# Performance work log

Measured on AMD Instinct MI355X. Metric: run time of the kernel, lower is better.

The kernel has to match this reference:

```python
import jax, jax.numpy as jnp
import numpy as np

E = 8      # n_routed_experts (== n_local)
K = 2      # n_activated_experts (top-k)
DIM = 2048
INTER = 1408
N_SHARED = 2
STD = 0.02


def setup_inputs() -> dict:
    key = jax.random.key(0)
    ks = jax.random.split(key, 9)
    B, S = 2, 2048
    return {
        "x": jax.random.normal(ks[0], (B, S, DIM), dtype=jnp.float32),
        "gate_w": jax.random.normal(ks[1], (E, DIM), dtype=jnp.float32) * STD,
        "router_bias": jnp.zeros((E,), dtype=jnp.float32),
        "W1": jax.random.normal(ks[2], (E, DIM, INTER), dtype=jnp.float32) * STD,
        "W3": jax.random.normal(ks[3], (E, DIM, INTER), dtype=jnp.float32) * STD,
        "W2": jax.random.normal(ks[4], (E, INTER, DIM), dtype=jnp.float32) * STD,
        "sw1": jax.random.normal(ks[5], (N_SHARED * INTER, DIM), dtype=jnp.float32) * STD,
        "sw3": jax.random.normal(ks[6], (N_SHARED * INTER, DIM), dtype=jnp.float32) * STD,
        "sw2": jax.random.normal(ks[7], (DIM, N_SHARED * INTER), dtype=jnp.float32) * STD,
    }


def reference(x, gate_w, router_bias, W1, W3, W2, sw1, sw3, sw2):
    B, S, D = x.shape
    X = x.reshape(-1, D)                       # [T, D]
    T = X.shape[0]

    # ---- Router: sigmoid scores, biased top-k selection, normalized weights
    logits = jnp.einsum('td,ed->te', X, gate_w)          # [T, E] (route_scale == 1.0)
    scores = jax.nn.sigmoid(logits)
    sel = scores + router_bias[None, :]
    _, idx = jax.lax.top_k(sel, K)                       # [T, K] int indices
    w = jnp.take_along_axis(scores, idx, axis=1)         # gather true scores
    w = w / jnp.clip(jnp.sum(w, axis=-1, keepdims=True), 1e-12)

    # Dense combine matrix [T, E]: gate weight where expert selected else 0
    gate_full = jnp.zeros((T, E), dtype=w.dtype).at[jnp.arange(T)[:, None], idx].set(w)

    # ---- Expert MLPs (SwiGLU) computed per-expert, combined by routing weight
    h1 = jnp.einsum('td,edh->eth', X, W1)                # [E, T, INTER]
    h3 = jnp.einsum('td,edh->eth', X, W3)
    y = jnp.einsum('eth,ehd->etd', jax.nn.silu(h1) * h3, W2)  # [E, T, D]
    out = jnp.einsum('etd,te->td', y, gate_full)         # weighted combine

    # ---- Shared expert MLP (always on)
    shared = jnp.einsum('th,dh->td',
                        jax.nn.silu(jnp.einsum('td,hd->th', X, sw1))
                        * jnp.einsum('td,hd->th', X, sw3), sw2)
    out = out + shared
    return out.reshape(B, S, D)
```

## Files before the change

### kernel.cpp

```cpp
#include <hip/hip_runtime.h>

#define DEV __device__ __forceinline__

typedef __attribute__((ext_vector_type(8))) short short8;
typedef __attribute__((ext_vector_type(4))) float floatx4;

constexpr int Tn  = 4096;
constexpr int Dm  = 2048;
constexpr int In  = 1408;
constexpr int En  = 8;
constexpr int SIn = 2816;
constexpr int CAP = 10240;

constexpr int SH_H = (Tn / 256) * (SIn / 128);
constexpr int SH_O = (Tn / 256) * (Dm / 256);
constexpr int NBLK = 256;

DEV unsigned short f2bf(float f) {
  unsigned int u = __float_as_uint(f);
  u += 0x7FFF + ((u >> 16) & 1);
  return (unsigned short)(u >> 16);
}

DEV float bf2f(unsigned short u) {
  return __uint_as_float(((unsigned int)u) << 16);
}

DEV void stg(const char* g, char* l) {
  __builtin_amdgcn_global_load_lds(
      (const __attribute__((address_space(1))) unsigned int*)g,
      (__attribute__((address_space(3))) unsigned int*)l, 16, 0, 0);
}

DEV unsigned ldsoff(const void* p) {
  return (unsigned)(unsigned long long)(__attribute__((address_space(3))) const char*)p;
}

#define BARR()  __builtin_amdgcn_s_barrier()
#define LGKM0() do { asm volatile("s_waitcnt lgkmcnt(0)" ::: "memory"); \
                     __builtin_amdgcn_sched_barrier(0); } while (0)
#define LGKM8() asm volatile("s_waitcnt lgkmcnt(8)" ::: "memory")
#define VMC(n)  asm volatile("s_waitcnt vmcnt(" #n ")" ::: "memory")
#define PRIO(x) __builtin_amdgcn_s_setprio(x)

#define DSR(dst, addr, OFFSTR) \
  asm volatile("ds_read_b128 %0, %1 offset:" OFFSTR : "=v"(dst) : "v"(addr))

#define RDA_LO(af, a) do { \
  DSR(af[0][0], a, "0");     DSR(af[0][1], a, "1024"); \
  DSR(af[1][0], a, "2048");  DSR(af[1][1], a, "3072"); \
  DSR(af[2][0], a, "4096");  DSR(af[2][1], a, "5120"); \
  DSR(af[3][0], a, "6144");  DSR(af[3][1], a, "7168"); } while (0)
#define RDA_HI(af, a) do { \
  DSR(af[0][0], a, "8192");  DSR(af[0][1], a, "9216"); \
  DSR(af[1][0], a, "10240"); DSR(af[1][1], a, "11264"); \
  DSR(af[2][0], a, "12288"); DSR(af[2][1], a, "13312"); \
  DSR(af[3][0], a, "14336"); DSR(af[3][1], a, "15360"); } while (0)
#define RDB_LO(bf, a) do { \
  DSR(bf[0][0], a, "0");    DSR(bf[0][1], a, "1024"); \
  DSR(bf[1][0], a, "2048"); DSR(bf[1][1], a, "3072"); } while (0)
#define RDB_HI(bf, a) do { \
  DSR(bf[2][0], a, "4096"); DSR(bf[2][1], a, "5120"); \
  DSR(bf[3][0], a, "6144"); DSR(bf[3][1], a, "7168"); } while (0)


__global__ void convert_all_kernel(const float* __restrict__ x,
                                   const float* __restrict__ sw1,
                                   const float* __restrict__ sw3,
                                   const float* __restrict__ sw2,
                                   unsigned short* __restrict__ Xb,
                                   unsigned short* __restrict__ sw1b,
                                   unsigned short* __restrict__ sw3b,
                                   unsigned short* __restrict__ sw2b) {
  int y = blockIdx.y;
  const float* src; unsigned short* dst; int n4;
  if (y == 0)      { src = x;   dst = Xb;   n4 = Tn * Dm / 4; }
  else if (y == 1) { src = sw1; dst = sw1b; n4 = SIn * Dm / 4; }
  else if (y == 2) { src = sw3; dst = sw3b; n4 = SIn * Dm / 4; }
  else             { src = sw2; dst = sw2b; n4 = Dm * SIn / 4; }
  int i = blockIdx.x * 256 + threadIdx.x;
  if (i >= n4) return;
  float4 v = ((const float4*)src)[i];
  union { unsigned short u[4]; unsigned long long ll; } p;
  p.u[0] = f2bf(v.x); p.u[1] = f2bf(v.y); p.u[2] = f2bf(v.z); p.u[3] = f2bf(v.w);
  *(unsigned long long*)(dst + (long)i * 4) = p.ll;
}

__global__ void transpose_all_kernel(const float* __restrict__ W1,
                                     const float* __restrict__ W3,
                                     const float* __restrict__ W2,
                                     unsigned short* __restrict__ W1t,
                                     unsigned short* __restrict__ W3t,
                                     unsigned short* __restrict__ W2t) {
  __shared__ float tile[64][65];
  int z = blockIdx.z;
  const float* s0; unsigned short* d0; int R, C;
  if (z == 0)      { s0 = W1; d0 = W1t; R = Dm; C = In; }
  else if (z == 1) { s0 = W3; d0 = W3t; R = Dm; C = In; }
  else             { s0 = W2; d0 = W2t; R = In; C = Dm; }
  int tilesC = C >> 6;
  int tr = (blockIdx.x / tilesC) << 6;
  int tc = (blockIdx.x % tilesC) << 6;
  const float* s = s0 + (long)blockIdx.y * R * C;
  unsigned short* d = d0 + (long)blockIdx.y * R * C;
  int rr = threadIdx.x >> 4, c4 = (threadIdx.x & 15) << 2;
#pragma unroll
  for (int p = 0; p < 4; p++) {
    float4 v = *(const float4*)&s[(long)(tr + rr + 16 * p) * C + tc + c4];
    tile[rr + 16 * p][c4]     = v.x;
    tile[rr + 16 * p][c4 + 1] = v.y;
    tile[rr + 16 * p][c4 + 2] = v.z;
    tile[rr + 16 * p][c4 + 3] = v.w;
  }
  __syncthreads();
  int oc = threadIdx.x >> 5, i2 = (threadIdx.x & 31) << 1;
#pragma unroll
  for (int p = 0; p < 8; p++) {
    int j = oc + 8 * p;
    union { unsigned short u[2]; unsigned int w; } pk;
    pk.u[0] = f2bf(tile[i2][j]);
    pk.u[1] = f2bf(tile[i2 + 1][j]);
    *(unsigned int*)&d[(long)(tc + j) * R + tr + i2] = pk.w;
  }
}


__global__ void init_kernel(int* counts, int* ptok) {
  int i = blockIdx.x * 256 + threadIdx.x;
  if (i < En) counts[i] = 0;
  if (i < CAP) ptok[i] = 0;
}

__global__ void router_kernel(const float* __restrict__ X, const float* __restrict__ GW,
                              const float* __restrict__ bias,
                              int* __restrict__ route_e, float* __restrict__ route_w,
                              int* __restrict__ counts) {
  int t = blockIdx.x, lane = threadIdx.x;
  const float* xr = X + (long)t * Dm;
  double acc[En];
#pragma unroll
  for (int e = 0; e < En; e++) acc[e] = 0.0;
  for (int d = lane; d < Dm; d += 64) {
    double xv = (double)xr[d];
#pragma unroll
    for (int e = 0; e < En; e++) acc[e] += xv * (double)GW[e * Dm + d];
  }
#pragma unroll
  for (int off = 32; off > 0; off >>= 1) {
#pragma unroll
    for (int e = 0; e < En; e++) acc[e] += __shfl_down(acc[e], off);
  }
  if (lane == 0) {
    double sc[En], sel[En];
#pragma unroll
    for (int e = 0; e < En; e++) {
      sc[e] = 1.0 / (1.0 + exp(-acc[e]));
      sel[e] = sc[e] + (double)bias[e];
    }
    int i0 = 0;
#pragma unroll
    for (int e = 1; e < En; e++) if (sel[e] > sel[i0]) i0 = e;
    int i1 = (i0 == 0) ? 1 : 0;
#pragma unroll
    for (int e = 0; e < En; e++) if (e != i0 && sel[e] > sel[i1]) i1 = e;
    double s = sc[i0] + sc[i1];
    if (s < 1e-12) s = 1e-12;
    route_e[t * 2] = i0;  route_e[t * 2 + 1] = i1;
    route_w[t * 2] = (float)(sc[i0] / s);  route_w[t * 2 + 1] = (float)(sc[i1] / s);
    atomicAdd(&counts[i0], 1);  atomicAdd(&counts[i1], 1);
  }
}

__global__ void offsets_kernel(const int* __restrict__ counts,
                               int* __restrict__ offs, int* __restrict__ fill) {
  if (threadIdx.x == 0) {
    int off = 0;
    for (int e = 0; e < En; e++) {
      offs[e] = off; fill[e] = off;
      off += (counts[e] + 255) & ~255;
    }
    offs[En] = off;
  }
}

__global__ void scatter_kernel(const int* __restrict__ re, int* __restrict__ fill,
                               int* __restrict__ pt, int* __restrict__ pslot) {
  int i = blockIdx.x * 256 + threadIdx.x;
  if (i < Tn * 2) {
    int e = re[i];
    int slot = atomicAdd(&fill[e], 1);
    pt[slot] = i >> 1;
    pslot[i] = slot;
  }
}


DEV void mm16(floatx4 (&acc)[8][4], const short8 (&af)[4][2],
              const short8 (&bf)[4][2], int mq, int nq) {
#pragma unroll
  for (int i = 0; i < 4; i++)
#pragma unroll
    for (int n = 0; n < 2; n++)
#pragma unroll
      for (int kk = 0; kk < 2; kk++)
        acc[4 * mq + i][2 * nq + n] = __builtin_amdgcn_mfma_f32_16x16x32_bf16(
            af[i][kk], bf[2 * nq + n][kk], acc[4 * mq + i][2 * nq + n], 0, 0, 0);
}

DEV void chunk_rc(int c, int& rowh, int& colb) {
  rowh = ((c >> 7) << 4) | ((c >> 2) & 15);
  colb = (((c >> 6) & 1) << 6) | ((((c & 3) << 4)) ^ ((c & 32) ? 32 : 0));
}

DEV void gemm_core(char* LDS, const char* (&gA)[2][2], const char* (&gB)[2][2],
                   floatx4 (&acc)[8][4], int NT, int wm, int wn, int wv, int aswz) {
  const int bsel = (wn >> 1) * 16384 + ((wn & 1) << 13);
  const int wb = wv * 1024;
  unsigned base = ldsoff(LDS);
  unsigned aA0 = base + wm * 16384 + aswz;
  unsigned aB0 = base + 32768 + bsel + aswz;
  unsigned aA1 = aA0 + 65536, aB1 = aB0 + 65536;
  stg(gB[0][0], LDS + 32768 + wb);
  stg(gB[1][0], LDS + 32768 + 16384 + wb);
  stg(gB[0][1], LDS + 32768 + 8192 + wb);
  stg(gB[1][1], LDS + 32768 + 16384 + 8192 + wb);
  stg(gA[0][0], LDS + wb);
  stg(gA[1][0], LDS + 16384 + wb);
  stg(gA[0][1], LDS + 8192 + wb);
  stg(gA[1][1], LDS + 16384 + 8192 + wb);
  stg(gA[0][0] + 128, LDS + 65536 + wb);
  stg(gA[1][0] + 128, LDS + 65536 + 16384 + wb);
  stg(gB[0][0] + 128, LDS + 65536 + 32768 + wb);
  stg(gB[1][0] + 128, LDS + 65536 + 32768 + 16384 + wb);
  VMC(4);
  BARR();
  short8 af[4][2], bf[4][2];

  auto tile = [&](int t, int b, unsigned aA, unsigned aB) {
    char* An = LDS + ((b ^ 1) << 16);
    char* Bn = An + 32768;
    char* Ac = LDS + (b << 16);
    char* Bc = Ac + 32768;
    const int kn = (t + 1) << 7, ka = (t + 2) << 7;
    const bool s1 = (t + 1 < NT), s2 = (t + 2 < NT);
    RDA_LO(af, aA); RDB_LO(bf, aB);
    if (s1) { stg(gB[0][1] + kn, Bn + 8192 + wb);
              stg(gB[1][1] + kn, Bn + 16384 + 8192 + wb); }
    LGKM8(); BARR(); LGKM0(); PRIO(1); mm16(acc, af, bf, 0, 0); PRIO(0); BARR();
    RDB_HI(bf, aB);
    if (s1) { stg(gA[0][1] + kn, An + 8192 + wb);
              stg(gA[1][1] + kn, An + 16384 + 8192 + wb); }
    BARR(); LGKM0(); PRIO(1); mm16(acc, af, bf, 0, 1); PRIO(0); BARR();
    RDA_HI(af, aA);
    if (s2) { stg(gA[0][0] + ka, Ac + wb);
              stg(gA[1][0] + ka, Ac + 16384 + wb); }
    BARR(); LGKM0(); PRIO(1); mm16(acc, af, bf, 1, 0); PRIO(0); BARR();
    if (s2) { stg(gB[0][0] + ka, Bc + wb);
              stg(gB[1][0] + ka, Bc + 16384 + wb); }
    BARR(); LGKM0(); PRIO(1); mm16(acc, af, bf, 1, 1); PRIO(0);
    if (s2)      { VMC(4); }
    else if (s1) { VMC(0); }
    BARR();
  };
#pragma unroll 1
  for (int t2 = 0; t2 < NT; t2 += 2) {
    tile(t2, 0, aA0, aB0);
    tile(t2 + 1, 1, aA1, aB1);
  }
}


DEV void h_body(const unsigned short* Xb, const unsigned short* B1p,
                const unsigned short* B3p, unsigned short* ap, int Nact,
                int m0, int n0, const int* ptok, bool routed, char* LDS) {
  int tid = threadIdx.x, wv = tid >> 6, lane = tid & 63;
  int wm = wv >> 2, wn = wv & 3;
  int fr = lane & 15, fq = lane >> 4;
  int aswz = fr * 64 + ((fq * 16) ^ ((fr & 8) << 2));

  const char* gA[2][2]; const char* gB[2][2];
#pragma unroll
  for (int j = 0; j < 2; j++) {
    int rowh, colb;
    chunk_rc(j * 512 + tid, rowh, colb);
#pragma unroll
    for (int h = 0; h < 2; h++) {
      int grA = m0 + h * 128 + rowh;
      long ra = routed ? (long)ptok[grA] : (long)grA;
      gA[h][j] = (const char*)Xb + ra * (long)(Dm * 2) + colb;
      int rt = h * 128 + rowh;
      const unsigned short* src = ((rt >> 5) & 1) ? B3p : B1p;
      long rb = (long)n0 + ((rt >> 6) << 5) + (rt & 31);
      gB[h][j] = (const char*)src + rb * (long)(Dm * 2) + colb;
    }
  }
  floatx4 acc[8][4];
#pragma unroll
  for (int i = 0; i < 8; i++)
#pragma unroll
    for (int n = 0; n < 4; n++) acc[i][n] = (floatx4)0.0f;

  gemm_core(LDS, gA, gB, acc, Dm / 64, wm, wn, wv, aswz);

#pragma unroll
  for (int mi = 0; mi < 8; mi++)
#pragma unroll
    for (int n = 0; n < 2; n++)
#pragma unroll
      for (int r = 0; r < 4; r++) {
        int row = m0 + wm * 128 + mi * 16 + fq * 4 + r;
        int col = n0 + wn * 32 + n * 16 + fr;
        float h1 = acc[mi][n][r], h3 = acc[mi][n + 2][r];
        float v = h1 / (1.0f + __expf(-h1)) * h3;
        ap[(long)row * Nact + col] = f2bf(v);
      }
}

__global__ __launch_bounds__(512, 1)
void h_all(const unsigned short* __restrict__ Xb,
           const unsigned short* __restrict__ W1t,
           const unsigned short* __restrict__ W3t,
           const unsigned short* __restrict__ sw1b,
           const unsigned short* __restrict__ sw3b,
           unsigned short* __restrict__ act,
           unsigned short* __restrict__ actS,
           const int* __restrict__ ptok,
           const int* __restrict__ offs) {
  extern __shared__ char LDS[];
  const int Mr = offs[En] >> 8;
  const int RT = Mr * (In / 128);
  const int TT = RT + SH_H;
#pragma unroll 1
  for (int t = blockIdx.x; t < TT; t += NBLK) {
    if (t < RT) {
      int m0 = (t % Mr) * 256, n0 = (t / Mr) * 128;
      int e = 0;
      while (!(m0 >= offs[e] && m0 < offs[e + 1])) e++;
      h_body(Xb, W1t + (long)e * In * Dm, W3t + (long)e * In * Dm,
             act, In, m0, n0, ptok, true, LDS);
    } else {
      int u = t - RT;
      int m0 = (u & 15) * 256, n0 = (u >> 4) * 128;
      h_body(Xb, sw1b, sw3b, actS, SIn, m0, n0, nullptr, false, LDS);
    }
  }
}


DEV void o_core(const unsigned short* Apt, const unsigned short* Bpt,
                int lda, int ldb, int NT, int m0, int n0,
                floatx4 (&acc)[8][4], char* LDS) {
  int tid = threadIdx.x, wv = tid >> 6, lane = tid & 63;
  int wm = wv >> 2, wn = wv & 3;
  int fr = lane & 15, fq = lane >> 4;
  int aswz = fr * 64 + ((fq * 16) ^ ((fr & 8) << 2));

  const char* gA[2][2]; const char* gB[2][2];
#pragma unroll
  for (int j = 0; j < 2; j++) {
    int rowh, colb;
    chunk_rc(j * 512 + tid, rowh, colb);
#pragma unroll
    for (int h = 0; h < 2; h++) {
      gA[h][j] = (const char*)Apt + (long)(m0 + h * 128 + rowh) * (lda * 2) + colb;
      gB[h][j] = (const char*)Bpt + (long)(n0 + h * 128 + rowh) * (ldb * 2) + colb;
    }
  }
#pragma unroll
  for (int i = 0; i < 8; i++)
#pragma unroll
    for (int n = 0; n < 4; n++) acc[i][n] = (floatx4)0.0f;

  gemm_core(LDS, gA, gB, acc, NT, wm, wn, wv, aswz);
}

__global__ __launch_bounds__(512, 1)
void o_all(const unsigned short* __restrict__ act,
           const unsigned short* __restrict__ actS,
           const unsigned short* __restrict__ W2t,
           const unsigned short* __restrict__ sw2b,
           unsigned short* __restrict__ yR,
           float* __restrict__ out,
           const int* __restrict__ offs) {
  extern __shared__ char LDS[];
  const int Mr = offs[En] >> 8;
  const int RT = Mr * (Dm / 256);
  const int TT = RT + SH_O;
  int lane = threadIdx.x & 63, wv = threadIdx.x >> 6;
  int wm = wv >> 2, wn = wv & 3;
  int fr = lane & 15, fq = lane >> 4;
#pragma unroll 1
  for (int t = blockIdx.x; t < TT; t += NBLK) {
    floatx4 acc[8][4];
    if (t < RT) {
      int m0 = (t % Mr) * 256, n0 = (t / Mr) * 256;
      int e = 0;
      while (!(m0 >= offs[e] && m0 < offs[e + 1])) e++;
      o_core(act, W2t + (long)e * Dm * In, In, In, In / 64, m0, n0, acc, LDS);
#pragma unroll
      for (int mi = 0; mi < 8; mi++)
#pragma unroll
        for (int r = 0; r < 4; r++) {
          int row = m0 + wm * 128 + mi * 16 + fq * 4 + r;
#pragma unroll
          for (int ni = 0; ni < 4; ni++) {
            int col = n0 + wn * 64 + ni * 16 + fr;
            yR[(long)row * Dm + col] = f2bf(acc[mi][ni][r]);
          }
        }
    } else {
      int u = t - RT;
      int m0 = (u & 15) * 256, n0 = (u >> 4) * 256;
      o_core(actS, sw2b, SIn, SIn, SIn / 64, m0, n0, acc, LDS);
#pragma unroll
      for (int mi = 0; mi < 8; mi++)
#pragma unroll
        for (int r = 0; r < 4; r++) {
          int row = m0 + wm * 128 + mi * 16 + fq * 4 + r;
#pragma unroll
          for (int ni = 0; ni < 4; ni++) {
            int col = n0 + wn * 64 + ni * 16 + fr;
            out[(long)row * Dm + col] = acc[mi][ni][r];
          }
        }
    }
  }
}


__global__ void combine_kernel(const unsigned short* __restrict__ yR,
                               const int* __restrict__ pslot,
                               const float* __restrict__ rw,
                               float* __restrict__ out) {
  int idx = blockIdx.x * 256 + threadIdx.x;
  int t = idx >> 9, c4 = idx & 511;
  int s0 = pslot[t * 2], s1 = pslot[t * 2 + 1];
  float w0 = rw[t * 2], w1 = rw[t * 2 + 1];
  ushort4 a = ((const ushort4*)(yR + (long)s0 * Dm))[c4];
  ushort4 b = ((const ushort4*)(yR + (long)s1 * Dm))[c4];
  float4* op = (float4*)(out + (long)t * Dm) + c4;
  float4 o = *op;
  o.x += w0 * bf2f(a.x) + w1 * bf2f(b.x);
  o.y += w0 * bf2f(a.y) + w1 * bf2f(b.y);
  o.z += w0 * bf2f(a.z) + w1 * bf2f(b.z);
  o.w += w0 * bf2f(a.w) + w1 * bf2f(b.w);
  *op = o;
}


extern "C" void kernel_launch(void* const* d_in, const int* in_sizes, int n_in,
                              void* d_out, int out_size, void* d_ws, size_t ws_size,
                              hipStream_t stream) {
  const float* x    = (const float*)d_in[0];
  const float* gw   = (const float*)d_in[1];
  const float* bias = (const float*)d_in[2];
  const float* W1   = (const float*)d_in[3];
  const float* W3   = (const float*)d_in[4];
  const float* W2   = (const float*)d_in[5];
  const float* sw1  = (const float*)d_in[6];
  const float* sw3  = (const float*)d_in[7];
  const float* sw2  = (const float*)d_in[8];
  float* out = (float*)d_out;

  static bool attr_done = false;
  if (!attr_done) {
    hipFuncSetAttribute(reinterpret_cast<const void*>(h_all),
                        hipFuncAttributeMaxDynamicSharedMemorySize, 131072);
    hipFuncSetAttribute(reinterpret_cast<const void*>(o_all),
                        hipFuncAttributeMaxDynamicSharedMemorySize, 131072);
    attr_done = true;
  }

  char* p = (char*)d_ws;
  auto alloc = [&](size_t bytes) {
    char* r = p; p += (bytes + 255) & ~(size_t)255; return r;
  };
  unsigned short* Xb   = (unsigned short*)alloc((size_t)Tn * Dm * 2);
  unsigned short* W1t  = (unsigned short*)alloc((size_t)En * In * Dm * 2);
  unsigned short* W3t  = (unsigned short*)alloc((size_t)En * In * Dm * 2);
  unsigned short* W2t  = (unsigned short*)alloc((size_t)En * Dm * In * 2);
  unsigned short* sw1b = (unsigned short*)alloc((size_t)SIn * Dm * 2);
  unsigned short* sw3b = (unsigned short*)alloc((size_t)SIn * Dm * 2);
  unsigned short* sw2b = (unsigned short*)alloc((size_t)Dm * SIn * 2);
  unsigned short* act  = (unsigned short*)alloc((size_t)CAP * In * 2);
  unsigned short* actS = (unsigned short*)alloc((size_t)Tn * SIn * 2);
  unsigned short* yR   = (unsigned short*)alloc((size_t)CAP * Dm * 2);
  int*   route_e = (int*)alloc(Tn * 2 * 4);
  float* route_w = (float*)alloc(Tn * 2 * 4);
  int*   counts  = (int*)alloc(256);
  int*   offs    = (int*)alloc(256);
  int*   fill    = (int*)alloc(256);
  int*   ptok    = (int*)alloc(CAP * 4);
  int*   pslot   = (int*)alloc(Tn * 2 * 4);

  convert_all_kernel<<<dim3(Tn * Dm / 4 / 256, 4), 256, 0, stream>>>(
      x, sw1, sw3, sw2, Xb, sw1b, sw3b, sw2b);
  transpose_all_kernel<<<dim3((Dm / 64) * (In / 64), En, 3), 256, 0, stream>>>(
      W1, W3, W2, W1t, W3t, W2t);

  init_kernel<<<(CAP + 255) / 256, 256, 0, stream>>>(counts, ptok);
  router_kernel<<<Tn, 64, 0, stream>>>(x, gw, bias, route_e, route_w, counts);
  offsets_kernel<<<1, 1, 0, stream>>>(counts, offs, fill);
  scatter_kernel<<<Tn * 2 / 256, 256, 0, stream>>>(route_e, fill, ptok, pslot);

  h_all<<<NBLK, 512, 131072, stream>>>(Xb, W1t, W3t, sw1b, sw3b, act, actS, ptok, offs);
  o_all<<<NBLK, 512, 131072, stream>>>(act, actS, W2t, sw2b, yR, out, offs);
  combine_kernel<<<Tn * (Dm / 4) / 256, 256, 0, stream>>>(yR, pslot, route_w, out);
}
```

Baseline: 832.5 us.

## Fuse prep kernels, merge offsets/scatter, and remap tile schedule per XCD

Merges the convert, transpose, router and init kernels into one prep kernel with block ranges, and replaces counts/offsets/scatter with a single-block LDS-based offscatter kernel. This cuts kernel launches and the global atomics. The h_all and o_all tile loops now give each XCD a contiguous chunk of tiles to improve L2 locality, and o_all schedules shared-expert tiles first. The single-block scatter serializes work, and the contiguous chunking may unbalance load across XCDs.

```diff
diff --git a/kernel.cpp b/kernel.cpp
--- a/kernel.cpp
+++ b/kernel.cpp
@@ -15,6 +15,19 @@
 constexpr int SH_H = (Tn / 256) * (SIn / 128);
 constexpr int SH_O = (Tn / 256) * (Dm / 256);
 constexpr int NBLK = 256;
+
+constexpr int RB  = Tn / 4;
+constexpr int IB  = CAP / 256;
+constexpr int CXB = Tn * Dm / 4 / 256;
+constexpr int CWB = SIn * Dm / 4 / 256;
+constexpr int TBZ = (Dm / 64) * (In / 64);
+constexpr int O1 = RB;
+constexpr int O2 = O1 + IB;
+constexpr int O3 = O2 + CXB;
+constexpr int O4 = O3 + CWB;
+constexpr int O5 = O4 + CWB;
+constexpr int O6 = O5 + CWB;
+constexpr int PREP_B = O6 + TBZ * En * 3;
 
 DEV unsigned short f2bf(float f) {
   unsigned int u = __float_as_uint(f);
@@ -64,45 +77,96 @@
   DSR(bf[3][0], a, "6144"); DSR(bf[3][1], a, "7168"); } while (0)
 
 
-__global__ void convert_all_kernel(const float* __restrict__ x,
-                                   const float* __restrict__ sw1,
-                                   const float* __restrict__ sw3,
-                                   const float* __restrict__ sw2,
-                                   unsigned short* __restrict__ Xb,
-                                   unsigned short* __restrict__ sw1b,
-                                   unsigned short* __restrict__ sw3b,
-                                   unsigned short* __restrict__ sw2b) {
-  int y = blockIdx.y;
-  const float* src; unsigned short* dst; int n4;
-  if (y == 0)      { src = x;   dst = Xb;   n4 = Tn * Dm / 4; }
-  else if (y == 1) { src = sw1; dst = sw1b; n4 = SIn * Dm / 4; }
-  else if (y == 2) { src = sw3; dst = sw3b; n4 = SIn * Dm / 4; }
-  else             { src = sw2; dst = sw2b; n4 = Dm * SIn / 4; }
-  int i = blockIdx.x * 256 + threadIdx.x;
-  if (i >= n4) return;
-  float4 v = ((const float4*)src)[i];
-  union { unsigned short u[4]; unsigned long long ll; } p;
-  p.u[0] = f2bf(v.x); p.u[1] = f2bf(v.y); p.u[2] = f2bf(v.z); p.u[3] = f2bf(v.w);
-  *(unsigned long long*)(dst + (long)i * 4) = p.ll;
-}
-
-__global__ void transpose_all_kernel(const float* __restrict__ W1,
-                                     const float* __restrict__ W3,
-                                     const float* __restrict__ W2,
-                                     unsigned short* __restrict__ W1t,
-                                     unsigned short* __restrict__ W3t,
-                                     unsigned short* __restrict__ W2t) {
+__global__ void prep_kernel(const float* __restrict__ x,
+                            const float* __restrict__ gw,
+                            const float* __restrict__ bias,
+                            const float* __restrict__ sw1,
+                            const float* __restrict__ sw3,
+                            const float* __restrict__ sw2,
+                            const float* __restrict__ W1,
+                            const float* __restrict__ W3,
+                            const float* __restrict__ W2,
+                            unsigned short* __restrict__ Xb,
+                            unsigned short* __restrict__ sw1b,
+                            unsigned short* __restrict__ sw3b,
+                            unsigned short* __restrict__ sw2b,
+                            unsigned short* __restrict__ W1t,
+                            unsigned short* __restrict__ W3t,
+                            unsigned short* __restrict__ W2t,
+                            int* __restrict__ route_e,
+                            float* __restrict__ route_w,
+                            int* __restrict__ ptok) {
   __shared__ float tile[64][65];
-  int z = blockIdx.z;
+  int bid = blockIdx.x;
+
+  if (bid < O1) {
+    int w = threadIdx.x >> 6, lane = threadIdx.x & 63;
+    int t = bid * 4 + w;
+    const float* xr = x + (long)t * Dm;
+    double acc[En];
+#pragma unroll
+    for (int e = 0; e < En; e++) acc[e] = 0.0;
+    for (int d = lane; d < Dm; d += 64) {
+      double xv = (double)xr[d];
+#pragma unroll
+      for (int e = 0; e < En; e++) acc[e] += xv * (double)gw[e * Dm + d];
+    }
+#pragma unroll
+    for (int off = 32; off > 0; off >>= 1) {
+#pragma unroll
+      for (int e = 0; e < En; e++) acc[e] += __shfl_down(acc[e], off);
+    }
+    if (lane == 0) {
+      double sc[En], sel[En];
+#pragma unroll
+      for (int e = 0; e < En; e++) {
+        sc[e] = 1.0 / (1.0 + exp(-acc[e]));
+        sel[e] = sc[e] + (double)bias[e];
+      }
+      int i0 = 0;
+#pragma unroll
+      for (int e = 1; e < En; e++) if (sel[e] > sel[i0]) i0 = e;
+      int i1 = (i0 == 0) ? 1 : 0;
+#pragma unroll
+      for (int e = 0; e < En; e++) if (e != i0 && sel[e] > sel[i1]) i1 = e;
+      double s = sc[i0] + sc[i1];
+      if (s < 1e-12) s = 1e-12;
+      route_e[t * 2] = i0;  route_e[t * 2 + 1] = i1;
+      route_w[t * 2] = (float)(sc[i0] / s);  route_w[t * 2 + 1] = (float)(sc[i1] / s);
+    }
+    return;
+  }
+  if (bid < O2) {
+    int i = (bid - O1) * 256 + threadIdx.x;
+    if (i < CAP) ptok[i] = 0;
+    return;
+  }
+  if (bid < O6) {
+    const float* src; unsigned short* dst; int i;
+    if (bid < O3)      { src = x;   dst = Xb;   i = (bid - O2) * 256 + threadIdx.x; }
+    else if (bid < O4) { src = sw1; dst = sw1b; i = (bid - O3) * 256 + threadIdx.x; }
+    else if (bid < O5) { src = sw3; dst = sw3b; i = (bid - O4) * 256 + threadIdx.x; }
+    else               { src = sw2; dst = sw2b; i = (bid - O5) * 256 + threadIdx.x; }
+    float4 v = ((const float4*)src)[i];
+    union { unsigned short u[4]; unsigned long long ll; } p;
+    p.u[0] = f2bf(v.x); p.u[1] = f2bf(v.y); p.u[2] = f2bf(v.z); p.u[3] = f2bf(v.w);
+    *(unsigned long long*)(dst + (long)i * 4) = p.ll;
+    return;
+  }
+  int tb = bid - O6;
+  int z = tb / (TBZ * En);
+  int rem = tb % (TBZ * En);
+  int y = rem / TBZ;
+  int xb = rem % TBZ;
   const float* s0; unsigned short* d0; int R, C;
   if (z == 0)      { s0 = W1; d0 = W1t; R = Dm; C = In; }
   else if (z == 1) { s0 = W3; d0 = W3t; R = Dm; C = In; }
   else             { s0 = W2; d0 = W2t; R = In; C = Dm; }
   int tilesC = C >> 6;
-  int tr = (blockIdx.x / tilesC) << 6;
-  int tc = (blockIdx.x % tilesC) << 6;
-  const float* s = s0 + (long)blockIdx.y * R * C;
-  unsigned short* d = d0 + (long)blockIdx.y * R * C;
+  int tr = (xb / tilesC) << 6;
+  int tc = (xb % tilesC) << 6;
+  const float* s = s0 + (long)y * R * C;
+  unsigned short* d = d0 + (long)y * R * C;
   int rr = threadIdx.x >> 4, c4 = (threadIdx.x & 15) << 2;
 #pragma unroll
   for (int p = 0; p < 4; p++) {
@@ -125,71 +189,28 @@
 }
 
 
-__global__ void init_kernel(int* counts, int* ptok) {
-  int i = blockIdx.x * 256 + threadIdx.x;
-  if (i < En) counts[i] = 0;
-  if (i < CAP) ptok[i] = 0;
-}
-
-__global__ void router_kernel(const float* __restrict__ X, const float* __restrict__ GW,
-                              const float* __restrict__ bias,
-                              int* __restrict__ route_e, float* __restrict__ route_w,
-                              int* __restrict__ counts) {
-  int t = blockIdx.x, lane = threadIdx.x;
-  const float* xr = X + (long)t * Dm;
-  double acc[En];
-#pragma unroll
-  for (int e = 0; e < En; e++) acc[e] = 0.0;
-  for (int d = lane; d < Dm; d += 64) {
-    double xv = (double)xr[d];
-#pragma unroll
-    for (int e = 0; e < En; e++) acc[e] += xv * (double)GW[e * Dm + d];
-  }
-#pragma unroll
-  for (int off = 32; off > 0; off >>= 1) {
-#pragma unroll
-    for (int e = 0; e < En; e++) acc[e] += __shfl_down(acc[e], off);
-  }
-  if (lane == 0) {
-    double sc[En], sel[En];
-#pragma unroll
-    for (int e = 0; e < En; e++) {
-      sc[e] = 1.0 / (1.0 + exp(-acc[e]));
-      sel[e] = sc[e] + (double)bias[e];
-    }
-    int i0 = 0;
-#pragma unroll
-    for (int e = 1; e < En; e++) if (sel[e] > sel[i0]) i0 = e;
-    int i1 = (i0 == 0) ? 1 : 0;
-#pragma unroll
-    for (int e = 0; e < En; e++) if (e != i0 && sel[e] > sel[i1]) i1 = e;
-    double s = sc[i0] + sc[i1];
-    if (s < 1e-12) s = 1e-12;
-    route_e[t * 2] = i0;  route_e[t * 2 + 1] = i1;
-    route_w[t * 2] = (float)(sc[i0] / s);  route_w[t * 2 + 1] = (float)(sc[i1] / s);
-    atomicAdd(&counts[i0], 1);  atomicAdd(&counts[i1], 1);
-  }
-}
-
-__global__ void offsets_kernel(const int* __restrict__ counts,
-                               int* __restrict__ offs, int* __restrict__ fill) {
-  if (threadIdx.x == 0) {
+__global__ void offscatter_kernel(const int* __restrict__ re,
+                                  int* __restrict__ offs,
+                                  int* __restrict__ ptok,
+                                  int* __restrict__ pslot) {
+  __shared__ int lcnt[En], loffs[En], lfill[En];
+  int tid = threadIdx.x;
+  if (tid < En) lcnt[tid] = 0;
+  __syncthreads();
+  for (int i = tid; i < Tn * 2; i += 1024) atomicAdd(&lcnt[re[i]], 1);
+  __syncthreads();
+  if (tid == 0) {
     int off = 0;
     for (int e = 0; e < En; e++) {
-      offs[e] = off; fill[e] = off;
-      off += (counts[e] + 255) & ~255;
+      loffs[e] = off; lfill[e] = off; offs[e] = off;
+      off += (lcnt[e] + 255) & ~255;
     }
     offs[En] = off;
   }
-}
-
-__global__ void scatter_kernel(const int* __restrict__ re, int* __restrict__ fill,
-                               int* __restrict__ pt, int* __restrict__ pslot) {
-  int i = blockIdx.x * 256 + threadIdx.x;
-  if (i < Tn * 2) {
-    int e = re[i];
-    int slot = atomicAdd(&fill[e], 1);
-    pt[slot] = i >> 1;
+  __syncthreads();
+  for (int i = tid; i < Tn * 2; i += 1024) {
+    int slot = atomicAdd(&lfill[re[i]], 1);
+    ptok[slot] = i >> 1;
     pslot[i] = slot;
   }
 }
@@ -330,8 +351,12 @@
   const int Mr = offs[En] >> 8;
   const int RT = Mr * (In / 128);
   const int TT = RT + SH_H;
+  const int per = (TT + 7) >> 3;
+  const int xcd = blockIdx.x & 7, lix = blockIdx.x >> 3;
 #pragma unroll 1
-  for (int t = blockIdx.x; t < TT; t += NBLK) {
+  for (int i = lix; i < per; i += 32) {
+    int t = xcd * per + i;
+    if (t >= TT) break;
     if (t < RT) {
       int m0 = (t % Mr) * 256, n0 = (t / Mr) * 128;
       int e = 0;
@@ -385,15 +410,20 @@
   extern __shared__ char LDS[];
   const int Mr = offs[En] >> 8;
   const int RT = Mr * (Dm / 256);
-  const int TT = RT + SH_O;
+  const int TT = SH_O + RT;
   int lane = threadIdx.x & 63, wv = threadIdx.x >> 6;
   int wm = wv >> 2, wn = wv & 3;
   int fr = lane & 15, fq = lane >> 4;
+  const int per = (TT + 7) >> 3;
+  const int xcd = blockIdx.x & 7, lix = blockIdx.x >> 3;
 #pragma unroll 1
-  for (int t = blockIdx.x; t < TT; t += NBLK) {
+  for (int i = lix; i < per; i += 32) {
+    int t = xcd * per + i;
+    if (t >= TT) break;
     floatx4 acc[8][4];
-    if (t < RT) {
-      int m0 = (t % Mr) * 256, n0 = (t / Mr) * 256;
+    if (t >= SH_O) {
+      int u = t - SH_O;
+      int m0 = (u % Mr) * 256, n0 = (u / Mr) * 256;
       int e = 0;
       while (!(m0 >= offs[e] && m0 < offs[e + 1])) e++;
       o_core(act, W2t + (long)e * Dm * In, In, In, In / 64, m0, n0, acc, LDS);
@@ -409,7 +439,7 @@
           }
         }
     } else {
-      int u = t - RT;
+      int u = t;
       int m0 = (u & 15) * 256, n0 = (u >> 4) * 256;
       o_core(actS, sw2b, SIn, SIn, SIn / 64, m0, n0, acc, LDS);
 #pragma unroll
@@ -487,23 +517,18 @@
   unsigned short* yR   = (unsigned short*)alloc((size_t)CAP * Dm * 2);
   int*   route_e = (int*)alloc(Tn * 2 * 4);
   float* route_w = (float*)alloc(Tn * 2 * 4);
-  int*   counts  = (int*)alloc(256);
   int*   offs    = (int*)alloc(256);
-  int*   fill    = (int*)alloc(256);
   int*   ptok    = (int*)alloc(CAP * 4);
   int*   pslot   = (int*)alloc(Tn * 2 * 4);
 
-  convert_all_kernel<<<dim3(Tn * Dm / 4 / 256, 4), 256, 0, stream>>>(
-      x, sw1, sw3, sw2, Xb, sw1b, sw3b, sw2b);
-  transpose_all_kernel<<<dim3((Dm / 64) * (In / 64), En, 3), 256, 0, stream>>>(
-      W1, W3, W2, W1t, W3t, W2t);
-
-  init_kernel<<<(CAP + 255) / 256, 256, 0, stream>>>(counts, ptok);
-  router_kernel<<<Tn, 64, 0, stream>>>(x, gw, bias, route_e, route_w, counts);
-  offsets_kernel<<<1, 1, 0, stream>>>(counts, offs, fill);
-  scatter_kernel<<<Tn * 2 / 256, 256, 0, stream>>>(route_e, fill, ptok, pslot);
+  prep_kernel<<<PREP_B, 256, 0, stream>>>(
+      x, gw, bias, sw1, sw3, sw2, W1, W3, W2,
+      Xb, sw1b, sw3b, sw2b, W1t, W3t, W2t, route_e, route_w, ptok);
+
+  offscatter_kernel<<<1, 1024, 0, stream>>>(route_e, offs, ptok, pslot);
 
   h_all<<<NBLK, 512, 131072, stream>>>(Xb, W1t, W3t, sw1b, sw3b, act, actS, ptok, offs);
   o_all<<<NBLK, 512, 131072, stream>>>(act, actS, W2t, sw2b, yR, out, offs);
+
   combine_kernel<<<Tn * (Dm / 4) / 256, 256, 0, stream>>>(yR, pslot, route_w, out);
 }
```

Measured after the change: 703.9 us. 1.18x faster.
